# Kernel tuning notes

Hardware: AMD Instinct MI355X
Metric: run time of the kernel (lower is better)

Reference implementation:

```python
import jax, jax.numpy as jnp
import numpy as np

B, S, R, E, H = 2, 256, 2048, 1024, 16
D = E // H
ROPE_BASE = 10000.0

_PN = ["sum_q", "sum_k", "sum_v", "sum_out", "reg_q", "reg_k", "reg_v", "reg_out", "sum_k2", "sum_v2"]


def setup_inputs() -> dict:
    key = jax.random.key(0)
    ks = jax.random.split(key, 2 + 2 * len(_PN))
    inp = {
        "sum_x": jax.random.normal(ks[0], (B, S, E), jnp.float32),
        "reg_x": jax.random.normal(ks[1], (B, R, E), jnp.float32),
        "ss_mask": jnp.ones((B, S, S), bool),
        "sr_mask": jnp.ones((B, S, R), bool),
        "rs_mask": jnp.ones((B, R, S), bool),
        "rr_mask": jnp.ones((B, R, R), bool),
    }
    for i, n in enumerate(_PN):
        inp[f"W_{n}"] = jax.random.normal(ks[2 + 2 * i], (E, E), jnp.float32) * 0.02
        inp[f"b_{n}"] = jax.random.normal(ks[3 + 2 * i], (E,), jnp.float32) * 0.02
    return inp


def _lin(x, W, b):
    return x @ W.T + b


def _heads(x):  # (B, L, E) -> (B, H, L, D)
    b, l, _ = x.shape
    return x.reshape(b, l, H, D).transpose(0, 2, 1, 3)


def _merge(x):  # (B, H, L, D) -> (B, L, E)
    b, _, l, _ = x.shape
    return x.transpose(0, 2, 1, 3).reshape(b, l, E)


def _rope_cos_sin(total_len):
    inv_freq = 1.0 / (ROPE_BASE ** (jnp.arange(0, D, 2, dtype=jnp.float32) / D))
    t = jnp.arange(total_len, dtype=jnp.float32)
    freqs = jnp.outer(t, inv_freq)
    emb = jnp.concatenate([freqs, freqs], axis=-1)  # (total_len, D)
    return jnp.cos(emb)[None, None], jnp.sin(emb)[None, None]


def _rotate_half(x):
    x1, x2 = jnp.split(x, 2, axis=-1)
    return jnp.concatenate([-x2, x1], axis=-1)


def _apply_rope(q, k, cos, sin):
    return q * cos + _rotate_half(q) * sin, k * cos + _rotate_half(k) * sin


def _attn(q, k, v, mask):  # mask: (B, Lq, Lk) bool
    scale = D ** -0.5
    scores = jnp.einsum('bhqd,bhkd->bhqk', q, k) * scale
    scores = jnp.where(mask[:, None, :, :], scores, -jnp.inf)
    p = jax.nn.softmax(scores, axis=-1)
    return jnp.einsum('bhqk,bhkd->bhqd', p, v)


def summary_attention(sum_x, reg_x, ss_mask, sr_mask, rs_mask, rr_mask, params):
    sum_len, reg_len = sum_x.shape[1], reg_x.shape[1]
    sum_q = _heads(_lin(sum_x, params["W_sum_q"], params["b_sum_q"]))
    sum_k = _heads(_lin(sum_x, params["W_sum_k"], params["b_sum_k"]))
    sum_v = _heads(_lin(sum_x, params["W_sum_v"], params["b_sum_v"]))
    reg_q = _heads(_lin(reg_x, params["W_reg_q"], params["b_reg_q"]))
    reg_k = _heads(_lin(reg_x, params["W_reg_k"], params["b_reg_k"]))
    reg_v = _heads(_lin(reg_x, params["W_reg_v"], params["b_reg_v"]))

    cos, sin = _rope_cos_sin(sum_len + reg_len)
    sum_q, sum_k = _apply_rope(sum_q, sum_k, cos[:, :, :sum_len], sin[:, :, :sum_len])
    reg_q, reg_k = _apply_rope(reg_q, reg_k, cos[:, :, sum_len:], sin[:, :, sum_len:])

    # Stage 1: summary queries over [summary, regular] keys
    src_k = jnp.concatenate([sum_k, reg_k], axis=2)
    src_v = jnp.concatenate([sum_v, reg_v], axis=2)
    sx_mask = jnp.concatenate([ss_mask, sr_mask], axis=-1)
    sum_attn_out = _merge(_attn(sum_q, src_k, src_v, sx_mask))  # (B, S, E)

    # Second projection of summarized tokens
    sum_k2 = _heads(_lin(sum_attn_out, params["W_sum_k2"], params["b_sum_k2"]))
    sum_v2 = _heads(_lin(sum_attn_out, params["W_sum_v2"], params["b_sum_v2"]))

    # Stage 2: regular queries over [summary2, regular] keys
    src_k2 = jnp.concatenate([sum_k2, reg_k], axis=2)
    src_v2 = jnp.concatenate([sum_v2, reg_v], axis=2)
    rx_mask = jnp.concatenate([rs_mask, rr_mask], axis=-1)
    reg_attn_out = _merge(_attn(reg_q, src_k2, src_v2, rx_mask))  # (B, R, E)

    sum_output = _lin(sum_attn_out, params["W_sum_out"], params["b_sum_out"])
    reg_output = _lin(reg_attn_out, params["W_reg_out"], params["b_reg_out"])
    return sum_output, reg_output


def reference(sum_x, reg_x, ss_mask, sr_mask, rs_mask, rr_mask,
              W_sum_q, b_sum_q, W_sum_k, b_sum_k, W_sum_v, b_sum_v,
              W_sum_out, b_sum_out, W_reg_q, b_reg_q, W_reg_k, b_reg_k,
              W_reg_v, b_reg_v, W_reg_out, b_reg_out, W_sum_k2, b_sum_k2,
              W_sum_v2, b_sum_v2):
    params = dict(W_sum_q=W_sum_q, b_sum_q=b_sum_q, W_sum_k=W_sum_k, b_sum_k=b_sum_k,
                  W_sum_v=W_sum_v, b_sum_v=b_sum_v, W_sum_out=W_sum_out, b_sum_out=b_sum_out,
                  W_reg_q=W_reg_q, b_reg_q=b_reg_q, W_reg_k=W_reg_k, b_reg_k=b_reg_k,
                  W_reg_v=W_reg_v, b_reg_v=b_reg_v, W_reg_out=W_reg_out, b_reg_out=b_reg_out,
                  W_sum_k2=W_sum_k2, b_sum_k2=b_sum_k2, W_sum_v2=W_sum_v2, b_sum_v2=b_sum_v2)
    return summary_attention(sum_x, reg_x, ss_mask, sr_mask, rs_mask, rr_mask, params)
```

## Files before the change

kernel.cpp:

```cpp
#include <hip/hip_runtime.h>
#include <math.h>

#define SUMSZ 524288
#define REGSZ 4194304
#define CSCALE 0.18033688f

typedef unsigned short us;
typedef __attribute__((ext_vector_type(8))) short short8;
typedef __attribute__((ext_vector_type(4))) float f32x4;

__device__ __forceinline__ us f2bf(float f) {
    unsigned u = __builtin_bit_cast(unsigned, f);
    u += 0x7FFF + ((u >> 16) & 1);
    return (us)(u >> 16);
}
__device__ __forceinline__ float fast_exp2(float x) {
    return __builtin_amdgcn_exp2f(x);
}
__device__ __forceinline__ unsigned pack_trunc(float a, float b, float& qa, float& qb) {
    unsigned ua = __builtin_bit_cast(unsigned, a);
    unsigned ub = __builtin_bit_cast(unsigned, b);
    qa = __builtin_bit_cast(float, ua & 0xffff0000u);
    qb = __builtin_bit_cast(float, ub & 0xffff0000u);
    return (ub & 0xffff0000u) | (ua >> 16);
}

struct GArgs {
    const us* A0; const us* A1;
    const us* W[6]; const float* bias[6]; void* C[6];
    int flag[6];
    int rope[6];
    float scale[6];
    const float* tab;
    int xsplit, Lmask0, Lmask1;
};

template<int BM, int BN, int NT>
__global__ __launch_bounds__(NT) void gemm6_kernel(GArgs a)
{
    constexpr int NWAVE = NT / 64;
    constexpr int WN = (NWAVE == 8) ? 4 : 2;
    constexpr int TI = BM / 16 / 2;
    constexpr int TJ = BN / 16 / WN;
    constexpr int AC = BM / (16 * NWAVE);
    constexpr int BC = BN / (16 * NWAVE);
    constexpr int CHROWS = 16 * NWAVE;
    const int tid = threadIdx.x;
    const int l = tid & 63, w = tid >> 6;
    const int col = l & 15, g = l >> 4;
    const int wm = w / WN, wn = w % WN;

    const int nwg = gridDim.x * gridDim.y;
    const int hw  = blockIdx.y * gridDim.x + blockIdx.x;
    const int q8  = nwg >> 3;
    const int flat = (hw & 7) * q8 + (hw >> 3);
    const int bx = flat / gridDim.y;
    const int by = flat % gridDim.y;

    const int part = (bx >= a.xsplit) ? 1 : 0;
    const int m0 = (part ? (bx - a.xsplit) : bx) * BM;
    const us* A = part ? a.A1 : a.A0;
    const int Lmask = part ? a.Lmask1 : a.Lmask0;
    const int nG = by * BN;
    const int set = part * 3 + (nG >> 10);
    const int n0 = nG & 1023;
    const us* W = a.W[set];
    const float* bias = a.bias[set];
    void* C = a.C[set];
    const int flag = a.flag[set];
    const int rope = a.rope[set];
    const float scl = a.scale[set];
    const float* tab = a.tab;

    __shared__ us As[2][(BM / 16) * 512];
    __shared__ us Bs[2][(BN / 16) * 512];

    f32x4 acc[TI][TJ];
    #pragma unroll
    for (int i = 0; i < TI; ++i)
        #pragma unroll
        for (int j = 0; j < TJ; ++j) acc[i][j] = (f32x4){0.f, 0.f, 0.f, 0.f};

    const us* ga = A + (size_t)(m0 + w * 16 + col) * 1024 + g * 8;
    const us* gb = W + (size_t)(n0 + w * 16 + col) * 1024 + g * 8;

    short8 pa[AC][2], pb[BC][2];
    auto ld = [&](int kt) {
        #pragma unroll
        for (int c = 0; c < AC; ++c) {
            pa[c][0] = *(const short8*)(ga + (size_t)c * CHROWS * 1024 + kt);
            pa[c][1] = *(const short8*)(ga + (size_t)c * CHROWS * 1024 + kt + 32);
        }
        #pragma unroll
        for (int c = 0; c < BC; ++c) {
            pb[c][0] = *(const short8*)(gb + (size_t)c * CHROWS * 1024 + kt);
            pb[c][1] = *(const short8*)(gb + (size_t)c * CHROWS * 1024 + kt + 32);
        }
    };
    ld(0);

    for (int kt = 0; kt < 1024; kt += 64) {
        __syncthreads();
        #pragma unroll
        for (int c = 0; c < AC; ++c) {
            *(short8*)&As[0][(w + NWAVE * c) * 512 + l * 8] = pa[c][0];
            *(short8*)&As[1][(w + NWAVE * c) * 512 + l * 8] = pa[c][1];
        }
        #pragma unroll
        for (int c = 0; c < BC; ++c) {
            *(short8*)&Bs[0][(w + NWAVE * c) * 512 + l * 8] = pb[c][0];
            *(short8*)&Bs[1][(w + NWAVE * c) * 512 + l * 8] = pb[c][1];
        }
        __syncthreads();
        if (kt + 64 < 1024) ld(kt + 64);

        #pragma unroll
        for (int hh = 0; hh < 2; ++hh) {
            short8 af[TI], bfr[TJ];
            #pragma unroll
            for (int i = 0; i < TI; ++i) af[i]  = *(const short8*)&As[hh][(wm * TI + i) * 512 + l * 8];
            #pragma unroll
            for (int j = 0; j < TJ; ++j) bfr[j] = *(const short8*)&Bs[hh][(wn * TJ + j) * 512 + l * 8];
            #pragma unroll
            for (int i = 0; i < TI; ++i)
                #pragma unroll
                for (int j = 0; j < TJ; ++j)
                    acc[i][j] = __builtin_amdgcn_mfma_f32_16x16x32_bf16(af[i], bfr[j], acc[i][j], 0, 0, 0);
        }
    }

    float bv[TJ];
    #pragma unroll
    for (int j = 0; j < TJ; ++j) bv[j] = bias[n0 + wn * (BN / WN) + j * 16 + col];
    #pragma unroll
    for (int i = 0; i < TI; ++i) {
        #pragma unroll
        for (int r = 0; r < 4; ++r) {
            int row = m0 + wm * (TI * 16) + i * 16 + g * 4 + r;
            float av[TJ];
            #pragma unroll
            for (int j = 0; j < TJ; ++j) av[j] = acc[i][j][r] + bv[j];
            if constexpr (TJ >= 4) {
                if (rope >= 0) {
                    int pos = (row & Lmask) + rope;
                    float c0 = tab[(pos * 32 + col) * 2],      s0 = tab[(pos * 32 + col) * 2 + 1];
                    float c1 = tab[(pos * 32 + col + 16) * 2], s1 = tab[(pos * 32 + col + 16) * 2 + 1];
                    #pragma unroll
                    for (int fb = 0; fb < TJ; fb += 4) {
                        float n0v = av[fb + 0] * c0 - av[fb + 2] * s0;
                        float n1v = av[fb + 1] * c1 - av[fb + 3] * s1;
                        float n2v = av[fb + 2] * c0 + av[fb + 0] * s0;
                        float n3v = av[fb + 3] * c1 + av[fb + 1] * s1;
                        av[fb + 0] = n0v; av[fb + 1] = n1v; av[fb + 2] = n2v; av[fb + 3] = n3v;
                    }
                }
            }
            #pragma unroll
            for (int j = 0; j < TJ; ++j) av[j] *= scl;
            size_t base = (size_t)row * 1024 + n0 + wn * (BN / WN) + col;
            if (flag) {
                us* Ch = (us*)C;
                #pragma unroll
                for (int j = 0; j < TJ; ++j) Ch[base + j * 16] = f2bf(av[j]);
            } else {
                float* Cf = (float*)C;
                #pragma unroll
                for (int j = 0; j < TJ; ++j) Cf[base + j * 16] = av[j];
            }
        }
    }
}

__global__ __launch_bounds__(256) void vtrans2_kernel(
    const us* __restrict__ src0, us* __restrict__ dst0, int L0, int xsplit,
    const us* __restrict__ src1, us* __restrict__ dst1, int L1)
{
    const int part = (blockIdx.x >= xsplit) ? 1 : 0;
    const int t = part ? (blockIdx.x - xsplit) : blockIdx.x;
    const us* src = part ? src1 : src0;
    us* dst = part ? dst1 : dst0;
    const int L = part ? L1 : L0;
    const int h = blockIdx.y, b = blockIdx.z;
    __shared__ us T[64][72];
    const int tid = threadIdx.x;
    {
        int key = tid >> 2, seg = (tid & 3) * 16;
        const us* sp = src + ((size_t)b * L + t * 64 + key) * 1024 + h * 64 + seg;
        short8 v0 = *(const short8*)sp;
        short8 v1 = *(const short8*)(sp + 8);
        int kp = (key & 15) * 4 + (key >> 4);
        #pragma unroll
        for (int j = 0; j < 8; ++j) {
            T[seg + j][kp]     = (us)v0[j];
            T[seg + 8 + j][kp] = (us)v1[j];
        }
    }
    __syncthreads();
    {
        int d = tid >> 2, ks = (tid & 3) * 16;
        us* dp = dst + (((size_t)(b * 16 + h) * 64) + d) * L + t * 64 + ks;
        *(short8*)dp       = *(const short8*)&T[d][ks];
        *(short8*)(dp + 8) = *(const short8*)&T[d][ks + 8];
    }
}

template<int NQ, int SPLIT, int NW>
__global__ __launch_bounds__(NW * 64) void attn5_kernel(
    const us* __restrict__ Q,
    const us* __restrict__ K1, const us* __restrict__ Vt1, int L1,
    const us* __restrict__ K2, const us* __restrict__ Vt2, int L2,
    us* __restrict__ O, float* __restrict__ PO, float* __restrict__ PL, int Lq)
{
    constexpr int CPW = 8 / NW;
    const int tid = threadIdx.x;
    const int l = tid & 63, w = tid >> 6;
    const int col = l & 15, g = l >> 4;

    const int GX = gridDim.x;
    const int flat = blockIdx.x + GX * (blockIdx.y + 16 * blockIdx.z);
    const int xcd = flat & 7;
    const int idx = flat >> 3;
    const int xq  = idx % GX;
    const int pair = xcd + 8 * (idx / GX);
    const int h = pair & 15, b = pair >> 4;
    const int split = xq & (SPLIT - 1);
    const int qt = xq / SPLIT;

    __shared__ us Ks[8 * 512];
    __shared__ us Vs[8 * 512];
    __shared__ us Ps[NW][NQ * 16 * 72];

    const int rowbase = qt * (NQ * 16 * NW) + w * (NQ * 16);

    short8 aq[NQ][2];
    #pragma unroll
    for (int qi = 0; qi < NQ; ++qi) {
        const us* qp = Q + ((size_t)b * Lq + rowbase + qi * 16 + col) * 1024 + h * 64 + g * 8;
        aq[qi][0] = *(const short8*)qp;
        aq[qi][1] = *(const short8*)(qp + 32);
    }

    f32x4 o[NQ][4];
    float lsum[NQ][4];
    #pragma unroll
    for (int qi = 0; qi < NQ; ++qi)
        #pragma unroll
        for (int u = 0; u < 4; ++u) { o[qi][u] = (f32x4){0.f,0.f,0.f,0.f}; lsum[qi][u] = 0.f; }

    const int nt1 = L1 >> 6;
    const int ntt = nt1 + (L2 >> 6);
    const int tpb = ntt / SPLIT;
    const int t0 = split * tpb, t1 = t0 + tpb;

    auto tload = [&](int t, short8* pk, short8* pv) {
        const us *Kg, *Vg; int Lv, kb;
        if (t < nt1) {
            Kg = K1 + ((size_t)b * L1 + t * 64) * 1024 + h * 64;
            Vg = Vt1 + (size_t)(b * 16 + h) * 64 * L1;
            Lv = L1; kb = t * 64;
        } else {
            Kg = K2 + ((size_t)b * L2 + (t - nt1) * 64) * 1024 + h * 64;
            Vg = Vt2 + (size_t)(b * 16 + h) * 64 * L2;
            Lv = L2; kb = (t - nt1) * 64;
        }
        #pragma unroll
        for (int c = 0; c < CPW; ++c) {
            int ci = w * CPW + c;
            pk[c] = *(const short8*)(Kg + (size_t)((ci >> 1) * 16 + col) * 1024 + (ci & 1) * 32 + g * 8);
            pv[c] = *(const short8*)(Vg + (size_t)((ci >> 1) * 16 + col) * Lv + kb + (ci & 1) * 32 + g * 8);
        }
    };

    short8 pk[CPW], pv[CPW];
    tload(t0, pk, pv);

    for (int t = t0; t < t1; ++t) {
        __syncthreads();
        #pragma unroll
        for (int c = 0; c < CPW; ++c) {
            *(short8*)&Ks[(w * CPW + c) * 512 + l * 8] = pk[c];
            *(short8*)&Vs[(w * CPW + c) * 512 + l * 8] = pv[c];
        }
        __syncthreads();
        if (t + 1 < t1) tload(t + 1, pk, pv);

        short8 kf[8], vb[8];
        #pragma unroll
        for (int f = 0; f < 8; ++f) kf[f] = *(const short8*)&Ks[f * 512 + l * 8];
        #pragma unroll
        for (int f = 0; f < 8; ++f) vb[f] = *(const short8*)&Vs[f * 512 + l * 8];

        #pragma unroll
        for (int qi = 0; qi < NQ; ++qi) {
            f32x4 s0 = {0.f,0.f,0.f,0.f}, s1 = s0, s2 = s0, s3 = s0;
            s0 = __builtin_amdgcn_mfma_f32_16x16x32_bf16(aq[qi][0], kf[0], s0, 0, 0, 0);
            s0 = __builtin_amdgcn_mfma_f32_16x16x32_bf16(aq[qi][1], kf[1], s0, 0, 0, 0);
            s1 = __builtin_amdgcn_mfma_f32_16x16x32_bf16(aq[qi][0], kf[2], s1, 0, 0, 0);
            s1 = __builtin_amdgcn_mfma_f32_16x16x32_bf16(aq[qi][1], kf[3], s1, 0, 0, 0);
            s2 = __builtin_amdgcn_mfma_f32_16x16x32_bf16(aq[qi][0], kf[4], s2, 0, 0, 0);
            s2 = __builtin_amdgcn_mfma_f32_16x16x32_bf16(aq[qi][1], kf[5], s2, 0, 0, 0);
            s3 = __builtin_amdgcn_mfma_f32_16x16x32_bf16(aq[qi][0], kf[6], s3, 0, 0, 0);
            s3 = __builtin_amdgcn_mfma_f32_16x16x32_bf16(aq[qi][1], kf[7], s3, 0, 0, 0);

            #pragma unroll
            for (int r = 0; r < 4; ++r) {
                float p0 = fast_exp2(s0[r]);
                float p1 = fast_exp2(s1[r]);
                float p2 = fast_exp2(s2[r]);
                float p3 = fast_exp2(s3[r]);
                float q0, q1, q2, q3;
                uint2 pkk;
                pkk.x = pack_trunc(p0, p1, q0, q1);
                pkk.y = pack_trunc(p2, p3, q2, q3);
                lsum[qi][r] += (q0 + q1) + (q2 + q3);
                *(uint2*)&Ps[w][(qi * 16 + g * 4 + r) * 72 + col * 4] = pkk;
            }
        }

        #pragma unroll
        for (int qi = 0; qi < NQ; ++qi) {
            short8 ap0 = *(const short8*)&Ps[w][(qi * 16 + col) * 72 + g * 8];
            short8 ap1 = *(const short8*)&Ps[w][(qi * 16 + col) * 72 + 32 + g * 8];
            o[qi][0] = __builtin_amdgcn_mfma_f32_16x16x32_bf16(ap0, vb[0], o[qi][0], 0, 0, 0);
            o[qi][0] = __builtin_amdgcn_mfma_f32_16x16x32_bf16(ap1, vb[1], o[qi][0], 0, 0, 0);
            o[qi][1] = __builtin_amdgcn_mfma_f32_16x16x32_bf16(ap0, vb[2], o[qi][1], 0, 0, 0);
            o[qi][1] = __builtin_amdgcn_mfma_f32_16x16x32_bf16(ap1, vb[3], o[qi][1], 0, 0, 0);
            o[qi][2] = __builtin_amdgcn_mfma_f32_16x16x32_bf16(ap0, vb[4], o[qi][2], 0, 0, 0);
            o[qi][2] = __builtin_amdgcn_mfma_f32_16x16x32_bf16(ap1, vb[5], o[qi][2], 0, 0, 0);
            o[qi][3] = __builtin_amdgcn_mfma_f32_16x16x32_bf16(ap0, vb[6], o[qi][3], 0, 0, 0);
            o[qi][3] = __builtin_amdgcn_mfma_f32_16x16x32_bf16(ap1, vb[7], o[qi][3], 0, 0, 0);
        }
    }

    #pragma unroll
    for (int qi = 0; qi < NQ; ++qi)
        #pragma unroll
        for (int r = 0; r < 4; ++r) {
            float v = lsum[qi][r];
            v += __shfl_xor(v, 1);
            v += __shfl_xor(v, 2);
            v += __shfl_xor(v, 4);
            v += __shfl_xor(v, 8);
            lsum[qi][r] = v;
        }

    if (SPLIT == 1) {
        #pragma unroll
        for (int qi = 0; qi < NQ; ++qi)
            #pragma unroll
            for (int r = 0; r < 4; ++r) {
                float inv = 1.0f / lsum[qi][r];
                size_t off = ((size_t)b * Lq + rowbase + qi * 16 + g * 4 + r) * 1024 + h * 64 + col;
                O[off]      = f2bf(o[qi][0][r] * inv);
                O[off + 16] = f2bf(o[qi][1][r] * inv);
                O[off + 32] = f2bf(o[qi][2][r] * inv);
                O[off + 48] = f2bf(o[qi][3][r] * inv);
            }
    } else {
        float* po = PO + (size_t)split * ((size_t)2 * Lq * 1024);
        float* pl = PL + split * (2 * Lq * 16);
        #pragma unroll
        for (int qi = 0; qi < NQ; ++qi)
            #pragma unroll
            for (int r = 0; r < 4; ++r) {
                int qr = rowbase + qi * 16 + g * 4 + r;
                size_t off = ((size_t)b * Lq + qr) * 1024 + h * 64 + col;
                po[off]      = o[qi][0][r];
                po[off + 16] = o[qi][1][r];
                po[off + 32] = o[qi][2][r];
                po[off + 48] = o[qi][3][r];
                if (col == 0) pl[(b * Lq + qr) * 16 + h] = lsum[qi][r];
            }
    }
}

__global__ __launch_bounds__(256) void combine_kernel(const float* __restrict__ po,
    const float* __restrict__ pl, us* __restrict__ out)
{
    int idx = blockIdx.x * 256 + threadIdx.x;
    int row = idx >> 10, c = idx & 1023, h = c >> 6;
    float lv = 0.f, ov = 0.f;
    #pragma unroll
    for (int s = 0; s < 4; ++s) {
        lv += pl[s * 8192 + row * 16 + h];
        ov += po[s * 524288 + idx];
    }
    out[idx] = f2bf(ov / lv);
}

__global__ __launch_bounds__(256) void cvt_flat_kernel(
    const float* s0, const float* s1, const float* s2, const float* s3,
    const float* s4, const float* s5, const float* s6, const float* s7,
    const float* s8, const float* s9, const float* s10, const float* s11,
    us* __restrict__ dst, float* __restrict__ tab)
{
    if (blockIdx.x >= 14848) {
        int idx = (blockIdx.x - 14848) * 256 + threadIdx.x;
        int pos = idx >> 5, j = idx & 31;
        float invf = fast_exp2((float)j * -0.41524101f);
        float ang = (float)pos * invf;
        float s, c;
        sincosf(ang, &s, &c);
        tab[idx * 2]     = c;
        tab[idx * 2 + 1] = s;
        return;
    }
    size_t e = (size_t)blockIdx.x * 1024 + threadIdx.x * 4;
    const float* src;
    size_t off;
    if (e < 10485760) {
        const float* ws[10] = {s0,s1,s2,s3,s4,s5,s6,s7,s8,s9};
        src = ws[e >> 20]; off = e & 1048575;
    } else if (e < 11010048) {
        src = s10; off = e - 10485760;
    } else {
        src = s11; off = e - 11010048;
    }
    float4 v = *(const float4*)(src + off);
    us o[4] = {f2bf(v.x), f2bf(v.y), f2bf(v.z), f2bf(v.w)};
    *(uint2*)(dst + e) = *(uint2*)o;
}

extern "C" void kernel_launch(void* const* d_in, const int* in_sizes, int n_in,
                              void* d_out, int out_size, void* d_ws, size_t ws_size,
                              hipStream_t stream)
{
    (void)in_sizes; (void)n_in; (void)out_size; (void)ws_size;

    const float* sum_x_f  = (const float*)d_in[0];
    const float* reg_x_f  = (const float*)d_in[1];
    const float* W_sum_q  = (const float*)d_in[6];  const float* b_sum_q  = (const float*)d_in[7];
    const float* W_sum_k  = (const float*)d_in[8];  const float* b_sum_k  = (const float*)d_in[9];
    const float* W_sum_v  = (const float*)d_in[10]; const float* b_sum_v  = (const float*)d_in[11];
    const float* W_sum_out= (const float*)d_in[12]; const float* b_sum_out= (const float*)d_in[13];
    const float* W_reg_q  = (const float*)d_in[14]; const float* b_reg_q  = (const float*)d_in[15];
    const float* W_reg_k  = (const float*)d_in[16]; const float* b_reg_k  = (const float*)d_in[17];
    const float* W_reg_v  = (const float*)d_in[18]; const float* b_reg_v  = (const float*)d_in[19];
    const float* W_reg_out= (const float*)d_in[20]; const float* b_reg_out= (const float*)d_in[21];
    const float* W_sum_k2 = (const float*)d_in[22]; const float* b_sum_k2 = (const float*)d_in[23];
    const float* W_sum_v2 = (const float*)d_in[24]; const float* b_sum_v2 = (const float*)d_in[25];

    float* out0 = (float*)d_out;
    float* out1 = out0 + SUMSZ;

    us* ws16     = (us*)d_ws;
    us* Wh       = ws16;
    us* xsh      = Wh + 10485760;
    us* xrh      = xsh + SUMSZ;
    us* sum_q    = xrh + REGSZ;
    us* sum_k    = sum_q + SUMSZ;
    us* sum_v    = sum_k + SUMSZ;
    us* sum_attn = sum_v + SUMSZ;
    us* sum_k2   = sum_attn + SUMSZ;
    us* sum_v2   = sum_k2 + SUMSZ;
    us* reg_q    = sum_v2 + SUMSZ;
    us* reg_k    = reg_q + REGSZ;
    us* reg_v    = reg_k + REGSZ;
    us* reg_attn = reg_v + REGSZ;
    us* VtS1     = reg_attn + REGSZ;
    float* tab   = (float*)(VtS1 + SUMSZ);
    float* po    = tab + 147456;
    float* pl    = po + 4 * 524288;
    us* VtR      = xrh;
    us* VtS2     = (us*)po;

    cvt_flat_kernel<<<15136, 256, 0, stream>>>(
        W_sum_q, W_sum_k, W_sum_v, W_sum_out, W_reg_q, W_reg_k, W_reg_v, W_reg_out,
        W_sum_k2, W_sum_v2, sum_x_f, reg_x_f, ws16, tab);

    {
        GArgs a{};
        a.A0 = xsh; a.A1 = xrh; a.xsplit = 2; a.Lmask0 = 255; a.Lmask1 = 2047;
        a.tab = tab;
        a.W[0] = Wh + 0u*1048576; a.bias[0] = b_sum_q; a.C[0] = sum_q; a.flag[0] = 1; a.rope[0] = 0;   a.scale[0] = 1.0f;
        a.W[1] = Wh + 1u*1048576; a.bias[1] = b_sum_k; a.C[1] = sum_k; a.flag[1] = 1; a.rope[1] = 0;   a.scale[1] = CSCALE;
        a.W[2] = Wh + 2u*1048576; a.bias[2] = b_sum_v; a.C[2] = sum_v; a.flag[2] = 1; a.rope[2] = -1;  a.scale[2] = 1.0f;
        a.W[3] = Wh + 4u*1048576; a.bias[3] = b_reg_q; a.C[3] = reg_q; a.flag[3] = 1; a.rope[3] = 256; a.scale[3] = 1.0f;
        a.W[4] = Wh + 5u*1048576; a.bias[4] = b_reg_k; a.C[4] = reg_k; a.flag[4] = 1; a.rope[4] = 256; a.scale[4] = CSCALE;
        a.W[5] = Wh + 6u*1048576; a.bias[5] = b_reg_v; a.C[5] = reg_v; a.flag[5] = 1; a.rope[5] = -1;  a.scale[5] = 1.0f;
        gemm6_kernel<256, 256, 512><<<dim3(18, 12), 512, 0, stream>>>(a);
    }

    vtrans2_kernel<<<dim3(36, 16, 2), 256, 0, stream>>>(
        sum_v, VtS1, 256, 4, reg_v, VtR, 2048);

    attn5_kernel<2, 4, 4><<<dim3(8, 16, 2), 256, 0, stream>>>(
        sum_q, sum_k, VtS1, 256, reg_k, VtR, 2048, nullptr, po, pl, 256);
    combine_kernel<<<2048, 256, 0, stream>>>(po, pl, sum_attn);

    {
        GArgs a{};
        a.A0 = sum_attn; a.A1 = sum_attn; a.xsplit = 8; a.Lmask0 = 255; a.Lmask1 = 255;
        a.tab = tab;
        a.W[0] = Wh + 8u*1048576; a.bias[0] = b_sum_k2; a.C[0] = sum_k2; a.flag[0] = 1; a.rope[0] = -1; a.scale[0] = CSCALE;
        a.W[1] = Wh + 9u*1048576; a.bias[1] = b_sum_v2; a.C[1] = sum_v2; a.flag[1] = 1; a.rope[1] = -1; a.scale[1] = 1.0f;
        a.W[2] = Wh + 3u*1048576; a.bias[2] = b_sum_out;a.C[2] = out0;   a.flag[2] = 0; a.rope[2] = -1; a.scale[2] = 1.0f;
        a.W[3] = a.W[0]; a.bias[3] = a.bias[0]; a.C[3] = a.C[0]; a.flag[3] = 1; a.rope[3] = -1; a.scale[3] = 1.0f;
        a.W[4] = a.W[0]; a.bias[4] = a.bias[0]; a.C[4] = a.C[0]; a.flag[4] = 1; a.rope[4] = -1; a.scale[4] = 1.0f;
        a.W[5] = a.W[0]; a.bias[5] = a.bias[0]; a.C[5] = a.C[0]; a.flag[5] = 1; a.rope[5] = -1; a.scale[5] = 1.0f;
        gemm6_kernel<64, 128, 256><<<dim3(8, 24), 256, 0, stream>>>(a);
    }

    vtrans2_kernel<<<dim3(4, 16, 2), 256, 0, stream>>>(
        sum_v2, VtS2, 256, 4, sum_v2, VtS2, 256);

    attn5_kernel<2, 1, 8><<<dim3(8, 16, 2), 512, 0, stream>>>(
        reg_q, sum_k2, VtS2, 256, reg_k, VtR, 2048, reg_attn, nullptr, nullptr, 2048);

    {
        GArgs a{};
        a.A0 = reg_attn; a.A1 = reg_attn; a.xsplit = 64; a.Lmask0 = 2047; a.Lmask1 = 2047;
        a.tab = tab;
        a.W[0] = Wh + 7u*1048576; a.bias[0] = b_reg_out; a.C[0] = out1; a.flag[0] = 0; a.rope[0] = -1; a.scale[0] = 1.0f;
        for (int s = 1; s < 6; ++s) {
            a.W[s] = a.W[0]; a.bias[s] = a.bias[0]; a.C[s] = a.C[0];
            a.flag[s] = 0; a.rope[s] = -1; a.scale[s] = 1.0f;
        }
        gemm6_kernel<64, 128, 256><<<dim3(64, 8), 256, 0, stream>>>(a);
    }
}
```

Baseline: 340.8 us.

## Process two KV tiles per barrier in reg attention and retile output GEMM

Adds a DEPTH template parameter to the attention kernel. K/V tiles are now staged in groups of DEPTH, so each pair of __syncthreads covers several 64-key tiles, with deeper register prefetch. It uses DEPTH=2 for the region attention and keeps 1 for the summary attention. The region output projection GEMM also moves to larger 128x128 tiles with 512 threads and a matching xsplit. The cost is doubled LDS and register footprint, which could lower occupancy, and if the tile count is odd the tail would run past t1.

```diff
diff --git a/kernel.cpp b/kernel.cpp
--- a/kernel.cpp
+++ b/kernel.cpp
@@ -204,7 +204,7 @@
     }
 }
 
-template<int NQ, int SPLIT, int NW>
+template<int NQ, int SPLIT, int NW, int DEPTH>
 __global__ __launch_bounds__(NW * 64) void attn5_kernel(
     const us* __restrict__ Q,
     const us* __restrict__ K1, const us* __restrict__ Vt1, int L1,
@@ -226,9 +226,9 @@
     const int split = xq & (SPLIT - 1);
     const int qt = xq / SPLIT;
 
-    __shared__ us Ks[8 * 512];
-    __shared__ us Vs[8 * 512];
-    __shared__ us Ps[NW][NQ * 16 * 72];
+    __shared__ us Ks[DEPTH][8 * 512];
+    __shared__ us Vs[DEPTH][8 * 512];
+    __shared__ us Ps[DEPTH][NW][NQ * 16 * 72];
 
     const int rowbase = qt * (NQ * 16 * NW) + w * (NQ * 16);
 
@@ -271,64 +271,73 @@
         }
     };
 
-    short8 pk[CPW], pv[CPW];
-    tload(t0, pk, pv);
-
-    for (int t = t0; t < t1; ++t) {
+    short8 pk[DEPTH][CPW], pv[DEPTH][CPW];
+    #pragma unroll
+    for (int d = 0; d < DEPTH; ++d) tload(t0 + d, pk[d], pv[d]);
+
+    for (int t = t0; t < t1; t += DEPTH) {
         __syncthreads();
         #pragma unroll
-        for (int c = 0; c < CPW; ++c) {
-            *(short8*)&Ks[(w * CPW + c) * 512 + l * 8] = pk[c];
-            *(short8*)&Vs[(w * CPW + c) * 512 + l * 8] = pv[c];
-        }
+        for (int d = 0; d < DEPTH; ++d)
+            #pragma unroll
+            for (int c = 0; c < CPW; ++c) {
+                *(short8*)&Ks[d][(w * CPW + c) * 512 + l * 8] = pk[d][c];
+                *(short8*)&Vs[d][(w * CPW + c) * 512 + l * 8] = pv[d][c];
+            }
         __syncthreads();
-        if (t + 1 < t1) tload(t + 1, pk, pv);
-
-        short8 kf[8], vb[8];
-        #pragma unroll
-        for (int f = 0; f < 8; ++f) kf[f] = *(const short8*)&Ks[f * 512 + l * 8];
-        #pragma unroll
-        for (int f = 0; f < 8; ++f) vb[f] = *(const short8*)&Vs[f * 512 + l * 8];
-
-        #pragma unroll
-        for (int qi = 0; qi < NQ; ++qi) {
-            f32x4 s0 = {0.f,0.f,0.f,0.f}, s1 = s0, s2 = s0, s3 = s0;
-            s0 = __builtin_amdgcn_mfma_f32_16x16x32_bf16(aq[qi][0], kf[0], s0, 0, 0, 0);
-            s0 = __builtin_amdgcn_mfma_f32_16x16x32_bf16(aq[qi][1], kf[1], s0, 0, 0, 0);
-            s1 = __builtin_amdgcn_mfma_f32_16x16x32_bf16(aq[qi][0], kf[2], s1, 0, 0, 0);
-            s1 = __builtin_amdgcn_mfma_f32_16x16x32_bf16(aq[qi][1], kf[3], s1, 0, 0, 0);
-            s2 = __builtin_amdgcn_mfma_f32_16x16x32_bf16(aq[qi][0], kf[4], s2, 0, 0, 0);
-            s2 = __builtin_amdgcn_mfma_f32_16x16x32_bf16(aq[qi][1], kf[5], s2, 0, 0, 0);
-            s3 = __builtin_amdgcn_mfma_f32_16x16x32_bf16(aq[qi][0], kf[6], s3, 0, 0, 0);
-            s3 = __builtin_amdgcn_mfma_f32_16x16x32_bf16(aq[qi][1], kf[7], s3, 0, 0, 0);
-
-            #pragma unroll
-            for (int r = 0; r < 4; ++r) {
-                float p0 = fast_exp2(s0[r]);
-                float p1 = fast_exp2(s1[r]);
-                float p2 = fast_exp2(s2[r]);
-                float p3 = fast_exp2(s3[r]);
-                float q0, q1, q2, q3;
-                uint2 pkk;
-                pkk.x = pack_trunc(p0, p1, q0, q1);
-                pkk.y = pack_trunc(p2, p3, q2, q3);
-                lsum[qi][r] += (q0 + q1) + (q2 + q3);
-                *(uint2*)&Ps[w][(qi * 16 + g * 4 + r) * 72 + col * 4] = pkk;
-            }
-        }
-
-        #pragma unroll
-        for (int qi = 0; qi < NQ; ++qi) {
-            short8 ap0 = *(const short8*)&Ps[w][(qi * 16 + col) * 72 + g * 8];
-            short8 ap1 = *(const short8*)&Ps[w][(qi * 16 + col) * 72 + 32 + g * 8];
-            o[qi][0] = __builtin_amdgcn_mfma_f32_16x16x32_bf16(ap0, vb[0], o[qi][0], 0, 0, 0);
-            o[qi][0] = __builtin_amdgcn_mfma_f32_16x16x32_bf16(ap1, vb[1], o[qi][0], 0, 0, 0);
-            o[qi][1] = __builtin_amdgcn_mfma_f32_16x16x32_bf16(ap0, vb[2], o[qi][1], 0, 0, 0);
-            o[qi][1] = __builtin_amdgcn_mfma_f32_16x16x32_bf16(ap1, vb[3], o[qi][1], 0, 0, 0);
-            o[qi][2] = __builtin_amdgcn_mfma_f32_16x16x32_bf16(ap0, vb[4], o[qi][2], 0, 0, 0);
-            o[qi][2] = __builtin_amdgcn_mfma_f32_16x16x32_bf16(ap1, vb[5], o[qi][2], 0, 0, 0);
-            o[qi][3] = __builtin_amdgcn_mfma_f32_16x16x32_bf16(ap0, vb[6], o[qi][3], 0, 0, 0);
-            o[qi][3] = __builtin_amdgcn_mfma_f32_16x16x32_bf16(ap1, vb[7], o[qi][3], 0, 0, 0);
+        if (t + DEPTH < t1) {
+            #pragma unroll
+            for (int d = 0; d < DEPTH; ++d) tload(t + DEPTH + d, pk[d], pv[d]);
+        }
+
+        #pragma unroll
+        for (int d = 0; d < DEPTH; ++d) {
+            short8 kf[8], vb[8];
+            #pragma unroll
+            for (int f = 0; f < 8; ++f) kf[f] = *(const short8*)&Ks[d][f * 512 + l * 8];
+            #pragma unroll
+            for (int f = 0; f < 8; ++f) vb[f] = *(const short8*)&Vs[d][f * 512 + l * 8];
+
+            #pragma unroll
+            for (int qi = 0; qi < NQ; ++qi) {
+                f32x4 s0 = {0.f,0.f,0.f,0.f}, s1 = s0, s2 = s0, s3 = s0;
+                s0 = __builtin_amdgcn_mfma_f32_16x16x32_bf16(aq[qi][0], kf[0], s0, 0, 0, 0);
+                s0 = __builtin_amdgcn_mfma_f32_16x16x32_bf16(aq[qi][1], kf[1], s0, 0, 0, 0);
+                s1 = __builtin_amdgcn_mfma_f32_16x16x32_bf16(aq[qi][0], kf[2], s1, 0, 0, 0);
+                s1 = __builtin_amdgcn_mfma_f32_16x16x32_bf16(aq[qi][1], kf[3], s1, 0, 0, 0);
+                s2 = __builtin_amdgcn_mfma_f32_16x16x32_bf16(aq[qi][0], kf[4], s2, 0, 0, 0);
+                s2 = __builtin_amdgcn_mfma_f32_16x16x32_bf16(aq[qi][1], kf[5], s2, 0, 0, 0);
+                s3 = __builtin_amdgcn_mfma_f32_16x16x32_bf16(aq[qi][0], kf[6], s3, 0, 0, 0);
+                s3 = __builtin_amdgcn_mfma_f32_16x16x32_bf16(aq[qi][1], kf[7], s3, 0, 0, 0);
+
+                #pragma unroll
+                for (int r = 0; r < 4; ++r) {
+                    float p0 = fast_exp2(s0[r]);
+                    float p1 = fast_exp2(s1[r]);
+                    float p2 = fast_exp2(s2[r]);
+                    float p3 = fast_exp2(s3[r]);
+                    float q0, q1, q2, q3;
+                    uint2 pkk;
+                    pkk.x = pack_trunc(p0, p1, q0, q1);
+                    pkk.y = pack_trunc(p2, p3, q2, q3);
+                    lsum[qi][r] += (q0 + q1) + (q2 + q3);
+                    *(uint2*)&Ps[d][w][(qi * 16 + g * 4 + r) * 72 + col * 4] = pkk;
+                }
+            }
+
+            #pragma unroll
+            for (int qi = 0; qi < NQ; ++qi) {
+                short8 ap0 = *(const short8*)&Ps[d][w][(qi * 16 + col) * 72 + g * 8];
+                short8 ap1 = *(const short8*)&Ps[d][w][(qi * 16 + col) * 72 + 32 + g * 8];
+                o[qi][0] = __builtin_amdgcn_mfma_f32_16x16x32_bf16(ap0, vb[0], o[qi][0], 0, 0, 0);
+                o[qi][0] = __builtin_amdgcn_mfma_f32_16x16x32_bf16(ap1, vb[1], o[qi][0], 0, 0, 0);
+                o[qi][1] = __builtin_amdgcn_mfma_f32_16x16x32_bf16(ap0, vb[2], o[qi][1], 0, 0, 0);
+                o[qi][1] = __builtin_amdgcn_mfma_f32_16x16x32_bf16(ap1, vb[3], o[qi][1], 0, 0, 0);
+                o[qi][2] = __builtin_amdgcn_mfma_f32_16x16x32_bf16(ap0, vb[4], o[qi][2], 0, 0, 0);
+                o[qi][2] = __builtin_amdgcn_mfma_f32_16x16x32_bf16(ap1, vb[5], o[qi][2], 0, 0, 0);
+                o[qi][3] = __builtin_amdgcn_mfma_f32_16x16x32_bf16(ap0, vb[6], o[qi][3], 0, 0, 0);
+                o[qi][3] = __builtin_amdgcn_mfma_f32_16x16x32_bf16(ap1, vb[7], o[qi][3], 0, 0, 0);
+            }
         }
     }
 
@@ -484,7 +493,7 @@
     vtrans2_kernel<<<dim3(36, 16, 2), 256, 0, stream>>>(
         sum_v, VtS1, 256, 4, reg_v, VtR, 2048);
 
-    attn5_kernel<2, 4, 4><<<dim3(8, 16, 2), 256, 0, stream>>>(
+    attn5_kernel<2, 4, 4, 1><<<dim3(8, 16, 2), 256, 0, stream>>>(
         sum_q, sum_k, VtS1, 256, reg_k, VtR, 2048, nullptr, po, pl, 256);
     combine_kernel<<<2048, 256, 0, stream>>>(po, pl, sum_attn);
 
@@ -504,18 +513,18 @@
     vtrans2_kernel<<<dim3(4, 16, 2), 256, 0, stream>>>(
         sum_v2, VtS2, 256, 4, sum_v2, VtS2, 256);
 
-    attn5_kernel<2, 1, 8><<<dim3(8, 16, 2), 512, 0, stream>>>(
+    attn5_kernel<2, 1, 8, 2><<<dim3(8, 16, 2), 512, 0, stream>>>(
         reg_q, sum_k2, VtS2, 256, reg_k, VtR, 2048, reg_attn, nullptr, nullptr, 2048);
 
     {
         GArgs a{};
-        a.A0 = reg_attn; a.A1 = reg_attn; a.xsplit = 64; a.Lmask0 = 2047; a.Lmask1 = 2047;
+        a.A0 = reg_attn; a.A1 = reg_attn; a.xsplit = 32; a.Lmask0 = 2047; a.Lmask1 = 2047;
         a.tab = tab;
         a.W[0] = Wh + 7u*1048576; a.bias[0] = b_reg_out; a.C[0] = out1; a.flag[0] = 0; a.rope[0] = -1; a.scale[0] = 1.0f;
         for (int s = 1; s < 6; ++s) {
             a.W[s] = a.W[0]; a.bias[s] = a.bias[0]; a.C[s] = a.C[0];
             a.flag[s] = 0; a.rope[s] = -1; a.scale[s] = 1.0f;
         }
-        gemm6_kernel<64, 128, 256><<<dim3(64, 8), 256, 0, stream>>>(a);
-    }
-}
+        gemm6_kernel<128, 128, 512><<<dim3(32, 8), 512, 0, stream>>>(a);
+    }
+}
```

Result: slower. 364.3 us (+6.9%).
